# Optimization experiments

Hardware: AMD Instinct MI355X
Metric: run time of the kernel (lower is better)

## Reference

```python
import jax, jax.numpy as jnp
import numpy as np

B, S, D, H, DH = 4, 2048, 1024, 16, 64
INIT_STD = 0.02
IGNORE = -100000.0


def setup_inputs() -> dict:
    key = jax.random.key(0)
    ks = jax.random.split(key, 5)
    x = jax.random.normal(ks[0], (B, S, D), dtype=jnp.float32)
    W_Q = INIT_STD * jax.random.normal(ks[1], (H, D, DH), dtype=jnp.float32)
    W_K = INIT_STD * jax.random.normal(ks[2], (H, D, DH), dtype=jnp.float32)
    W_V = INIT_STD * jax.random.normal(ks[3], (H, D, DH), dtype=jnp.float32)
    W_O = INIT_STD * jax.random.normal(ks[4], (H, DH, D), dtype=jnp.float32)
    b_Q = jnp.zeros((H, DH), dtype=jnp.float32)
    b_K = jnp.zeros((H, DH), dtype=jnp.float32)
    b_V = jnp.zeros((H, DH), dtype=jnp.float32)
    b_O = jnp.zeros((D,), dtype=jnp.float32)
    return {"x": x, "W_Q": W_Q, "b_Q": b_Q, "W_K": W_K, "b_K": b_K,
            "W_V": W_V, "b_V": b_V, "W_O": W_O, "b_O": b_O}


def reference(x, W_Q, b_Q, W_K, b_K, W_V, b_V, W_O, b_O):
    # x: (B, S, D); projections -> (B, S, H, DH)
    Q = jnp.einsum('bqd,hde->bqhe', x, W_Q) + b_Q
    K = jnp.einsum('bkd,hde->bkhe', x, W_K) + b_K
    V = jnp.einsum('bkd,hde->bkhe', x, W_V) + b_V
    d_head = Q.shape[-1]
    # scores: (B, H, Sq, Sk)
    scores = jnp.einsum('bqhe,bkhe->bhqk', Q, K) / np.sqrt(d_head).astype(np.float32)
    s = scores.shape[-1]
    causal = jnp.triu(jnp.ones((s, s), dtype=bool), k=1)
    scores = jnp.where(causal, jnp.float32(IGNORE), scores)
    A = jax.nn.softmax(scores, axis=-1)
    z = jnp.einsum('bhqk,bkhe->bqhe', A, V)
    # output projection: sum over heads + bias
    attn_out = jnp.einsum('bqhe,hed->bqd', z, W_O) + b_O
    return attn_out
```

## Files before the change

kernel.cpp:

```cpp
#include <hip/hip_runtime.h>


#define B_ 4
#define S_ 2048
#define D_ 1024
#define H_ 16
#define DH_ 64

typedef unsigned short ushort_t;
typedef __attribute__((ext_vector_type(4))) short short4v;
typedef __attribute__((ext_vector_type(8))) short short8v;
typedef __attribute__((ext_vector_type(4))) float floatx4;
typedef __attribute__((ext_vector_type(4))) unsigned short ushort4v;

static __device__ __forceinline__ ushort_t f2bf(float f) {
    union { float f; unsigned u; } v; v.f = f;
    unsigned r = v.u + 0x7fffu + ((v.u >> 16) & 1u);
    return (ushort_t)(r >> 16);
}

static __device__ __forceinline__ float fast_exp2(float x) {
#if __has_builtin(__builtin_amdgcn_exp2f)
    return __builtin_amdgcn_exp2f(x);
#else
    return exp2f(x);
#endif
}

static __device__ __forceinline__ unsigned pack_bf16_tr(float lo, float hi) {
    union { float f; unsigned u; } a, b;
    a.f = lo; b.f = hi;
    return __builtin_amdgcn_perm(b.u, a.u, 0x07060302u);
}

static __device__ __forceinline__ void g2lds16(const void* g, void* l) {
    __builtin_amdgcn_global_load_lds(
        (__attribute__((address_space(1))) void*)(unsigned long long)(size_t)g,
        (__attribute__((address_space(3))) void*)(unsigned int)(size_t)l,
        16, 0, 0);
}

__global__ void prep_kernel(const float* __restrict__ x,
                            const float* __restrict__ wq, const float* __restrict__ wk,
                            const float* __restrict__ wv, const float* __restrict__ wo,
                            ushort_t* __restrict__ xb, ushort_t* __restrict__ wt,
                            ushort_t* __restrict__ wot) {
    __shared__ float tile[32][33];
    int bid = blockIdx.x;
    int tid = threadIdx.x;
    if (bid < 8192) {
        int i = (bid * 256 + tid) * 4;
        float4 v = *(const float4*)&x[i];
        ushort4v o;
        o[0] = f2bf(v.x); o[1] = f2bf(v.y); o[2] = f2bf(v.z); o[3] = f2bf(v.w);
        *(ushort4v*)&xb[i] = o;
        return;
    }
    const float* src;
    ushort_t* d;
    int C, r0, c0;
    if (bid < 11264) {
        int t = bid - 8192;
        int z = t / 64, r = t % 64;
        src = (z < 16 ? wq : (z < 32 ? wk : wv)) + (size_t)(z & 15) * 65536;
        d = wt + (size_t)z * 65536;
        C = 64; r0 = (r >> 1) * 32; c0 = (r & 1) * 32;
    } else {
        int t = bid - 11264;
        int z = t / 64, r = t % 64;
        src = wo + (size_t)z * 65536;
        d = wot + (size_t)z * 64;
        C = 1024; r0 = (r & 1) * 32; c0 = (r >> 1) * 32;
    }
    int tx = tid & 31, ty = tid >> 5;
#pragma unroll
    for (int i = 0; i < 4; ++i)
        tile[ty + i * 8][tx] = src[(size_t)(r0 + ty + i * 8) * C + c0 + tx];
    __syncthreads();
#pragma unroll
    for (int i = 0; i < 4; ++i)
        d[(size_t)(c0 + ty + i * 8) * 1024 + r0 + tx] = f2bf(tile[tx][ty + i * 8]);
}


#define GQ_BAR() __builtin_amdgcn_s_barrier()
#define GQ_VM4 do { asm volatile("s_waitcnt vmcnt(4)"); __builtin_amdgcn_sched_barrier(0); } while (0)
#define GQ_VM1 do { asm volatile("s_waitcnt vmcnt(1)"); __builtin_amdgcn_sched_barrier(0); } while (0)
#define GQ_VM0 do { asm volatile("s_waitcnt vmcnt(0)"); __builtin_amdgcn_sched_barrier(0); } while (0)
#define GQ_WAITLG do { asm volatile("s_waitcnt lgkmcnt(0)"); __builtin_amdgcn_sched_barrier(0); } while (0)

#define GQ_READS_B(KB)                                                          \
    _Pragma("unroll") for (int nt = 0; nt < 4; ++nt)                            \
        bfr[KB][nt] = *(const short8v*)&cB[(wn * 64 + nt * 16) * 64 + ((KB) ? kb1 : kb0)];

#define GQ_READS_A(MH, KB)                                                      \
    _Pragma("unroll") for (int i = 0; i < 2; ++i)                               \
        af[i] = *(const short8v*)&cA[(wm * 64 + ((MH) * 2 + i) * 16) * 64 + ((KB) ? kb1 : kb0)];

#define GQ_MFMA(MH, KB)                                                         \
    GQ_WAITLG;                                                                  \
    __builtin_amdgcn_s_setprio(1);                                              \
    _Pragma("unroll") for (int i = 0; i < 2; ++i)                               \
        _Pragma("unroll") for (int nt = 0; nt < 4; ++nt)                        \
            acc[(MH) * 2 + i][nt] = __builtin_amdgcn_mfma_f32_16x16x32_bf16(    \
                af[i], bfr[KB][nt], acc[(MH) * 2 + i][nt], 0, 0, 0);            \
    __builtin_amdgcn_s_setprio(0);                                              \
    __builtin_amdgcn_sched_barrier(0);

#define GQ_KSTEP(CA, CB, S1, S2, S3, S4, WMID, WEND) do {                       \
    const ushort_t* cA = (CA); const ushort_t* cB = (CB);                       \
    short8v af[2]; short8v bfr[2][4];                                           \
    GQ_READS_B(0) GQ_READS_A(0, 0) S1; GQ_BAR();                                \
    GQ_MFMA(0, 0) GQ_BAR();                                                     \
    GQ_READS_B(1) GQ_READS_A(0, 1) S2; GQ_BAR();                                \
    GQ_MFMA(0, 1) WMID; GQ_BAR();                                               \
    GQ_READS_A(1, 0) S3; GQ_BAR();                                              \
    GQ_MFMA(1, 0) GQ_BAR();                                                     \
    GQ_READS_A(1, 1) S4; GQ_BAR();                                              \
    GQ_MFMA(1, 1) WEND; GQ_BAR();                                               \
} while (0)

#define GQ_BODY(APTR, BPTR)                                                     \
    stageA1(sA[0], 0, uRA);                                                     \
    stageB1(sB[0], 0, w * 32);                                                  \
    stageB1(sB[0], 0, w * 32 + 8);                                              \
    stageB1(sB[0], 0, w * 32 + 16);                                             \
    stageB1(sB[0], 0, w * 32 + 24);                                             \
    stageA1(sA[0], 0, uRA + 32);                                                \
    GQ_VM1;                                                                     \
    GQ_BAR();                                                                   \
    int p = 0;                                                                  \
    for (int t = 0; t < 15; ++t) {                                              \
        const int kk = (t + 1) * 64;                                            \
        ushort_t* nA = sA[p ^ 1];                                               \
        ushort_t* nB = sB[p ^ 1];                                               \
        GQ_KSTEP(sA[p], sB[p],                                                  \
                 { stageA1(nA, kk, uRA); stageB1(nB, kk, w * 32); },            \
                 { stageB1(nB, kk, w * 32 + 8); stageB1(nB, kk, w * 32 + 16); },\
                 { stageB1(nB, kk, w * 32 + 24); },                             \
                 { stageA1(nA, kk, uRA + 32); },                                \
                 GQ_VM4, GQ_VM1);                                               \
        p ^= 1;                                                                 \
    }                                                                           \
    GQ_KSTEP(sA[1], sB[1], (void)0, (void)0, (void)0, (void)0, GQ_VM0, (void)0);

__global__ __launch_bounds__(512, 2) void gemm_qkv(const ushort_t* __restrict__ A,
                                                   const ushort_t* __restrict__ Wt,
                                                   const float* __restrict__ bq,
                                                   const float* __restrict__ bk,
                                                   const float* __restrict__ bv,
                                                   ushort_t* __restrict__ Qw,
                                                   ushort_t* __restrict__ Kw,
                                                   ushort_t* __restrict__ Vw) {
    __shared__ ushort_t sA[2][128 * 64];
    __shared__ ushort_t sB[2][256 * 64];
    const int tid = threadIdx.x;
    const int lane = tid & 63, w = tid >> 6;
    const int lq = lane & 15, quad = lane >> 4;
    const int wm = w >> 2, wn = w & 3;
    const int m0 = blockIdx.x * 128, n0 = blockIdx.y * 256;

    const int kb0 = lq * 64 + ((quad ^ (lq & 7)) << 3);
    const int kb1 = lq * 64 + (((4 | quad) ^ (lq & 7)) << 3);

    const int uRA = ((w >> 2) << 6) + (w & 3) * 8;

    auto stageA1 = [&](ushort_t* dst, int kk, int R0) __attribute__((always_inline)) {
        int rr = R0 + (lane >> 3);
        int cc = (lane & 7) ^ (rr & 7);
        g2lds16(&A[(size_t)(m0 + rr) * 1024 + kk + cc * 8], &dst[R0 * 64]);
    };
    auto stageB1 = [&](ushort_t* dst, int kk, int R0) __attribute__((always_inline)) {
        int rr = R0 + (lane >> 3);
        int cc = (lane & 7) ^ (rr & 7);
        g2lds16(&Wt[(size_t)(n0 + rr) * 1024 + kk + cc * 8], &dst[R0 * 64]);
    };

    floatx4 acc[4][4] = {};

    GQ_BODY(A, Wt)

    const int mat = blockIdx.y >> 2;
    const float* bias = mat == 0 ? bq : (mat == 1 ? bk : bv);
    const int colbase = (blockIdx.y & 3) * 256 + wn * 64;
    float bias_v[4];
#pragma unroll
    for (int nt = 0; nt < 4; ++nt) bias_v[nt] = bias[colbase + nt * 16 + lq];

#pragma unroll
    for (int mt = 0; mt < 4; ++mt) {
#pragma unroll
        for (int nt = 0; nt < 4; ++nt) {
            int row0 = m0 + wm * 64 + mt * 16 + quad * 4;
            int col = colbase + nt * 16 + lq;
            int h = col >> 6, e = col & 63;
            if (mat == 2) {
                int b = row0 >> 11, s = row0 & 2047;
                ushort4v pk;
#pragma unroll
                for (int rg = 0; rg < 4; ++rg) pk[rg] = f2bf(acc[mt][nt][rg] + bias_v[nt]);
                *(ushort4v*)&Vw[((size_t)((b << 4) | h) * 64 + e) * 2048 + s] = pk;
            } else {
                ushort_t* Du = mat == 0 ? Qw : Kw;
#pragma unroll
                for (int rg = 0; rg < 4; ++rg) {
                    int row = row0 + rg;
                    int b = row >> 11, s = row & 2047;
                    float v = acc[mt][nt][rg] + bias_v[nt];
                    if (mat == 0) v *= 0.18033688011112042f;
                    Du[((size_t)((b << 4) | h) * 2048 + s) * 64 + e] = f2bf(v);
                }
            }
        }
    }
}

#define VROW 140
__global__ __launch_bounds__(256, 3) void attn_kernel(const ushort_t* __restrict__ Q,
                                                      const ushort_t* __restrict__ Kg,
                                                      const ushort_t* __restrict__ Vt,
                                                      ushort_t* __restrict__ Z) {
    __shared__ ushort_t sK[2][128 * 64];
    __shared__ ushort_t sV[64 * VROW];
    const int tid = threadIdx.x;
    const int lane = tid & 63, w = tid >> 6;
    const int lq = lane & 15, quad = lane >> 4;
    const int bh = blockIdx.x;
    const int b = bh >> 4, h = bh & 15;
    const ushort_t* Qp = Q + (size_t)bh * S_ * DH_;
    const ushort_t* Kp = Kg + (size_t)bh * S_ * DH_;
    const ushort_t* Vp = Vt + (size_t)bh * DH_ * S_;

    const int kbase0 = lq * 64 + ((quad ^ (lq & 7)) << 3);
    const int kbase1 = lq * 64 + (((4 | quad) ^ (lq & 7)) << 3);
    const int vbase = lq * VROW + quad * 4;
    const int vr = w * 16 + (lane >> 2);
    const int vc = (lane & 3) * 32;

    const floatx4 fzero = {0.f, 0.f, 0.f, 0.f};

    auto stageK = [&](int kt, int bs) __attribute__((always_inline)) {
        ushort_t* dK = sK[bs];
#pragma unroll
        for (int p = 0; p < 4; ++p) {
            int rrk = w * 32 + p * 8 + (lane >> 3);
            int ck = (lane & 7) ^ (rrk & 7);
            g2lds16(&Kp[(size_t)(kt * 128 + rrk) * 64 + ck * 8], &dK[(w * 32 + p * 8) * 64]);
        }
    };
    auto loadV = [&](int kt, short8v* vr4) __attribute__((always_inline)) {
        const ushort_t* src = &Vp[(size_t)vr * 2048 + kt * 128 + vc];
#pragma unroll
        for (int j = 0; j < 4; ++j) vr4[j] = *(const short8v*)&src[j * 8];
    };
    auto writeV = [&](const short8v* vr4) __attribute__((always_inline)) {
        ushort_t* dst = &sV[vr * VROW + vc];
#pragma unroll
        for (int j = 0; j < 4; ++j) *(short8v*)&dst[j * 8] = vr4[j];
    };

    const int qt = 15 - (int)blockIdx.y;
    const int q0 = qt * 128;

    short8v qf[2][2];
#pragma unroll
    for (int qi = 0; qi < 2; ++qi)
#pragma unroll
        for (int ks = 0; ks < 2; ++ks)
            qf[qi][ks] = *(const short8v*)&Qp[(size_t)(q0 + w * 32 + qi * 16 + lq) * DH_ + ks * 32 + quad * 8];

    float l_i[2] = {0.f, 0.f};
    floatx4 o[2][4] = {};
    short8v vreg[4];

    stageK(0, 0);
    loadV(0, vreg);

    for (int kt = 0; kt <= qt; ++kt) {
        const bool diag = (kt == qt);
        const ushort_t* cK = sK[kt & 1];

        __syncthreads();
        writeV(vreg);
        if (kt < qt) {
            stageK(kt + 1, (kt + 1) & 1);
            loadV(kt + 1, vreg);
        }

        floatx4 st[8][2];
#pragma unroll
        for (int si = 0; si < 8; ++si) {
            short8v a0 = *(const short8v*)&cK[kbase0 + si * 1024];
            short8v a1 = *(const short8v*)&cK[kbase1 + si * 1024];
#pragma unroll
            for (int qi = 0; qi < 2; ++qi) {
                st[si][qi] = __builtin_amdgcn_mfma_f32_16x16x32_bf16(a0, qf[qi][0], fzero, 0, 0, 0);
                st[si][qi] = __builtin_amdgcn_mfma_f32_16x16x32_bf16(a1, qf[qi][1], st[si][qi], 0, 0, 0);
            }
        }

        short4v pf[8][2];
#pragma unroll
        for (int qi = 0; qi < 2; ++qi) {
            const int qg = q0 + w * 32 + qi * 16 + lq;
            float lsum = 0.f;
#pragma unroll
            for (int si = 0; si < 8; ++si) {
                float p[4];
#pragma unroll
                for (int rg = 0; rg < 4; ++rg) {
                    float v = st[si][qi][rg];
                    if (diag) {
                        int sg = kt * 128 + si * 16 + quad * 4 + rg;
                        if (sg > qg) v = -1e30f;
                    }
                    p[rg] = fast_exp2(v);
                    lsum += p[rg];
                }
                union { unsigned u[2]; short4v v4; } pk;
                pk.u[0] = pack_bf16_tr(p[0], p[1]);
                pk.u[1] = pack_bf16_tr(p[2], p[3]);
                pf[si][qi] = pk.v4;
            }
            l_i[qi] += lsum;
        }

        __syncthreads();

#pragma unroll
        for (int ksp = 0; ksp < 8; ++ksp) {
#pragma unroll
            for (int et = 0; et < 4; ++et) {
                short4v vf = *(const short4v*)&sV[vbase + et * (16 * VROW) + ksp * 16];
#pragma unroll
                for (int qi = 0; qi < 2; ++qi)
                    o[qi][et] = __builtin_amdgcn_mfma_f32_16x16x16bf16_1k(pf[ksp][qi], vf, o[qi][et], 0, 0, 0);
            }
        }
    }

#pragma unroll
    for (int qi = 0; qi < 2; ++qi) {
        float lf = l_i[qi];
        lf += __shfl_xor(lf, 16);
        lf += __shfl_xor(lf, 32);
        float linv[4];
#pragma unroll
        for (int rg = 0; rg < 4; ++rg) linv[rg] = 1.0f / __shfl(lf, quad * 4 + rg);
#pragma unroll
        for (int et = 0; et < 4; ++et) {
#pragma unroll
            for (int rg = 0; rg < 4; ++rg) {
                int qg = q0 + w * 32 + qi * 16 + quad * 4 + rg;
                int e = et * 16 + lq;
                Z[((size_t)(b * S_ + qg) * H_ + h) * DH_ + e] = f2bf(o[qi][et][rg] * linv[rg]);
            }
        }
    }
}

__global__ __launch_bounds__(512, 2) void gemm_o(const ushort_t* __restrict__ A,
                                                 const ushort_t* __restrict__ Bt,
                                                 const float* __restrict__ bias,
                                                 float* __restrict__ Dst) {
    __shared__ ushort_t sA[2][128 * 64];
    __shared__ ushort_t sB[2][256 * 64];
    const int tid = threadIdx.x;
    const int lane = tid & 63, w = tid >> 6;
    const int lq = lane & 15, quad = lane >> 4;
    const int wm = w >> 2, wn = w & 3;
    const int m0 = blockIdx.x * 128, n0 = blockIdx.y * 256;

    const int kb0 = lq * 64 + ((quad ^ (lq & 7)) << 3);
    const int kb1 = lq * 64 + (((4 | quad) ^ (lq & 7)) << 3);
    const int uRA = ((w >> 2) << 6) + (w & 3) * 8;

    auto stageA1 = [&](ushort_t* dst, int kk, int R0) __attribute__((always_inline)) {
        int rr = R0 + (lane >> 3);
        int cc = (lane & 7) ^ (rr & 7);
        g2lds16(&A[(size_t)(m0 + rr) * 1024 + kk + cc * 8], &dst[R0 * 64]);
    };
    auto stageB1 = [&](ushort_t* dst, int kk, int R0) __attribute__((always_inline)) {
        int rr = R0 + (lane >> 3);
        int cc = (lane & 7) ^ (rr & 7);
        g2lds16(&Bt[(size_t)(n0 + rr) * 1024 + kk + cc * 8], &dst[R0 * 64]);
    };

    floatx4 acc[4][4] = {};

    GQ_BODY(A, Bt)

    const int colbase = n0 + wn * 64;
    float bias_v[4];
#pragma unroll
    for (int nt = 0; nt < 4; ++nt) bias_v[nt] = bias[colbase + nt * 16 + lq];

#pragma unroll
    for (int mt = 0; mt < 4; ++mt) {
#pragma unroll
        for (int nt = 0; nt < 4; ++nt) {
            int row0 = m0 + wm * 64 + mt * 16 + quad * 4;
            int col = colbase + nt * 16 + lq;
#pragma unroll
            for (int rg = 0; rg < 4; ++rg)
                Dst[(size_t)(row0 + rg) * 1024 + col] = acc[mt][nt][rg] + bias_v[nt];
        }
    }
}

extern "C" void kernel_launch(void* const* d_in, const int* in_sizes, int n_in,
                              void* d_out, int out_size, void* d_ws, size_t ws_size,
                              hipStream_t stream) {
    const float* x  = (const float*)d_in[0];
    const float* wq = (const float*)d_in[1];
    const float* bq = (const float*)d_in[2];
    const float* wk = (const float*)d_in[3];
    const float* bk = (const float*)d_in[4];
    const float* wv = (const float*)d_in[5];
    const float* bv = (const float*)d_in[6];
    const float* wo = (const float*)d_in[7];
    const float* bo = (const float*)d_in[8];

    char* ws = (char*)d_ws;
    size_t off = 0;
    ushort_t* xb  = (ushort_t*)(ws + off); off += (size_t)8192 * 1024 * 2;
    ushort_t* wt  = (ushort_t*)(ws + off); off += (size_t)3 * 1024 * 1024 * 2;
    ushort_t* wot = (ushort_t*)(ws + off); off += (size_t)1024 * 1024 * 2;
    ushort_t* Qw  = (ushort_t*)(ws + off); off += (size_t)8192 * 1024 * 2;
    ushort_t* Kw  = (ushort_t*)(ws + off); off += (size_t)8192 * 1024 * 2;
    ushort_t* Vw  = (ushort_t*)(ws + off); off += (size_t)8192 * 1024 * 2;
    ushort_t* Zw  = (ushort_t*)(ws + off); off += (size_t)8192 * 1024 * 2;

    prep_kernel<<<12288, 256, 0, stream>>>(x, wq, wk, wv, wo, xb, wt, wot);
    gemm_qkv<<<dim3(64, 12), 512, 0, stream>>>(xb, wt, bq, bk, bv, Qw, Kw, Vw);
    attn_kernel<<<dim3(64, 16), 256, 0, stream>>>(Qw, Kw, Vw, Zw);
    gemm_o<<<dim3(64, 4), 512, 0, stream>>>(Zw, wot, bo, (float*)d_out);
}
```

Measured before the change: 295.8 us.

## Shrink GEMM tiles to 128x128 and pair causal query tiles in attention

Both projection GEMMs move from 512-thread 128x256 tiles to 256-thread 128x128 tiles, doubling the grid and adjusting the staging and waitcnt bookkeeping. The attention kernel now processes two complementary query tiles per block (qt and 15-qt) to balance causal work, halving the grid. V is staged through async global-to-LDS copies into a double-buffered, XOR-swizzled layout instead of a register round trip into a padded array, which removes one barrier per iteration. The changes trade per-block work size and occupancy against load balance and more tile-level reuse of global loads.

```diff
diff --git a/kernel.cpp b/kernel.cpp
--- a/kernel.cpp
+++ b/kernel.cpp
@@ -85,7 +85,7 @@
 
 #define GQ_BAR() __builtin_amdgcn_s_barrier()
 #define GQ_VM4 do { asm volatile("s_waitcnt vmcnt(4)"); __builtin_amdgcn_sched_barrier(0); } while (0)
-#define GQ_VM1 do { asm volatile("s_waitcnt vmcnt(1)"); __builtin_amdgcn_sched_barrier(0); } while (0)
+#define GQ_VM2 do { asm volatile("s_waitcnt vmcnt(2)"); __builtin_amdgcn_sched_barrier(0); } while (0)
 #define GQ_VM0 do { asm volatile("s_waitcnt vmcnt(0)"); __builtin_amdgcn_sched_barrier(0); } while (0)
 #define GQ_WAITLG do { asm volatile("s_waitcnt lgkmcnt(0)"); __builtin_amdgcn_sched_barrier(0); } while (0)
 
@@ -120,14 +120,12 @@
     GQ_MFMA(1, 1) WEND; GQ_BAR();                                               \
 } while (0)
 
-#define GQ_BODY(APTR, BPTR)                                                     \
-    stageA1(sA[0], 0, uRA);                                                     \
-    stageB1(sB[0], 0, w * 32);                                                  \
-    stageB1(sB[0], 0, w * 32 + 8);                                              \
-    stageB1(sB[0], 0, w * 32 + 16);                                             \
-    stageB1(sB[0], 0, w * 32 + 24);                                             \
-    stageA1(sA[0], 0, uRA + 32);                                                \
-    GQ_VM1;                                                                     \
+#define GQ_RUN()                                                                \
+    stA(sA[0], 0, uA); stA(sA[0], 0, uA + 8);                                   \
+    stB(sB[0], 0, bR); stB(sB[0], 0, bR + 8);                                   \
+    stB(sB[0], 0, bR + 16); stB(sB[0], 0, bR + 24);                             \
+    stA(sA[0], 0, uA + 32); stA(sA[0], 0, uA + 40);                             \
+    GQ_VM2;                                                                     \
     GQ_BAR();                                                                   \
     int p = 0;                                                                  \
     for (int t = 0; t < 15; ++t) {                                              \
@@ -135,16 +133,16 @@
         ushort_t* nA = sA[p ^ 1];                                               \
         ushort_t* nB = sB[p ^ 1];                                               \
         GQ_KSTEP(sA[p], sB[p],                                                  \
-                 { stageA1(nA, kk, uRA); stageB1(nB, kk, w * 32); },            \
-                 { stageB1(nB, kk, w * 32 + 8); stageB1(nB, kk, w * 32 + 16); },\
-                 { stageB1(nB, kk, w * 32 + 24); },                             \
-                 { stageA1(nA, kk, uRA + 32); },                                \
-                 GQ_VM4, GQ_VM1);                                               \
+                 { stA(nA, kk, uA); stA(nA, kk, uA + 8); },                     \
+                 { stB(nB, kk, bR); stB(nB, kk, bR + 8); },                     \
+                 { stB(nB, kk, bR + 16); stB(nB, kk, bR + 24); },               \
+                 { stA(nA, kk, uA + 32); stA(nA, kk, uA + 40); },               \
+                 GQ_VM4, GQ_VM2);                                               \
         p ^= 1;                                                                 \
     }                                                                           \
     GQ_KSTEP(sA[1], sB[1], (void)0, (void)0, (void)0, (void)0, GQ_VM0, (void)0);
 
-__global__ __launch_bounds__(512, 2) void gemm_qkv(const ushort_t* __restrict__ A,
+__global__ __launch_bounds__(256, 2) void gemm_qkv(const ushort_t* __restrict__ A,
                                                    const ushort_t* __restrict__ Wt,
                                                    const float* __restrict__ bq,
                                                    const float* __restrict__ bk,
@@ -153,24 +151,25 @@
                                                    ushort_t* __restrict__ Kw,
                                                    ushort_t* __restrict__ Vw) {
     __shared__ ushort_t sA[2][128 * 64];
-    __shared__ ushort_t sB[2][256 * 64];
+    __shared__ ushort_t sB[2][128 * 64];
     const int tid = threadIdx.x;
     const int lane = tid & 63, w = tid >> 6;
     const int lq = lane & 15, quad = lane >> 4;
-    const int wm = w >> 2, wn = w & 3;
-    const int m0 = blockIdx.x * 128, n0 = blockIdx.y * 256;
+    const int wm = w >> 1, wn = w & 1;
+    const int m0 = blockIdx.x * 128, n0 = blockIdx.y * 128;
 
     const int kb0 = lq * 64 + ((quad ^ (lq & 7)) << 3);
     const int kb1 = lq * 64 + (((4 | quad) ^ (lq & 7)) << 3);
 
-    const int uRA = ((w >> 2) << 6) + (w & 3) * 8;
-
-    auto stageA1 = [&](ushort_t* dst, int kk, int R0) __attribute__((always_inline)) {
+    const int uA = ((w >> 1) << 6) + ((w & 1) << 4);
+    const int bR = w * 32;
+
+    auto stA = [&](ushort_t* dst, int kk, int R0) __attribute__((always_inline)) {
         int rr = R0 + (lane >> 3);
         int cc = (lane & 7) ^ (rr & 7);
         g2lds16(&A[(size_t)(m0 + rr) * 1024 + kk + cc * 8], &dst[R0 * 64]);
     };
-    auto stageB1 = [&](ushort_t* dst, int kk, int R0) __attribute__((always_inline)) {
+    auto stB = [&](ushort_t* dst, int kk, int R0) __attribute__((always_inline)) {
         int rr = R0 + (lane >> 3);
         int cc = (lane & 7) ^ (rr & 7);
         g2lds16(&Wt[(size_t)(n0 + rr) * 1024 + kk + cc * 8], &dst[R0 * 64]);
@@ -178,11 +177,11 @@
 
     floatx4 acc[4][4] = {};
 
-    GQ_BODY(A, Wt)
-
-    const int mat = blockIdx.y >> 2;
+    GQ_RUN()
+
+    const int mat = blockIdx.y >> 3;
     const float* bias = mat == 0 ? bq : (mat == 1 ? bk : bv);
-    const int colbase = (blockIdx.y & 3) * 256 + wn * 64;
+    const int colbase = (blockIdx.y & 7) * 128 + wn * 64;
     float bias_v[4];
 #pragma unroll
     for (int nt = 0; nt < 4; ++nt) bias_v[nt] = bias[colbase + nt * 16 + lq];
@@ -215,13 +214,12 @@
     }
 }
 
-#define VROW 140
-__global__ __launch_bounds__(256, 3) void attn_kernel(const ushort_t* __restrict__ Q,
-                                                      const ushort_t* __restrict__ Kg,
-                                                      const ushort_t* __restrict__ Vt,
-                                                      ushort_t* __restrict__ Z) {
+__global__ __launch_bounds__(256) void attn_kernel(const ushort_t* __restrict__ Q,
+                                                   const ushort_t* __restrict__ Kg,
+                                                   const ushort_t* __restrict__ Vt,
+                                                   ushort_t* __restrict__ Z) {
     __shared__ ushort_t sK[2][128 * 64];
-    __shared__ ushort_t sV[64 * VROW];
+    __shared__ ushort_t sV[2][64 * 128];
     const int tid = threadIdx.x;
     const int lane = tid & 63, w = tid >> 6;
     const int lq = lane & 15, quad = lane >> 4;
@@ -233,9 +231,8 @@
 
     const int kbase0 = lq * 64 + ((quad ^ (lq & 7)) << 3);
     const int kbase1 = lq * 64 + (((4 | quad) ^ (lq & 7)) << 3);
-    const int vbase = lq * VROW + quad * 4;
-    const int vr = w * 16 + (lane >> 2);
-    const int vc = (lane & 3) * 32;
+    const int vbase2 = lq * 128 + quad * 4;
+    const int vko = (lq & 7) << 4;
 
     const floatx4 fzero = {0.f, 0.f, 0.f, 0.f};
 
@@ -248,139 +245,142 @@
             g2lds16(&Kp[(size_t)(kt * 128 + rrk) * 64 + ck * 8], &dK[(w * 32 + p * 8) * 64]);
         }
     };
-    auto loadV = [&](int kt, short8v* vr4) __attribute__((always_inline)) {
-        const ushort_t* src = &Vp[(size_t)vr * 2048 + kt * 128 + vc];
-#pragma unroll
-        for (int j = 0; j < 4; ++j) vr4[j] = *(const short8v*)&src[j * 8];
-    };
-    auto writeV = [&](const short8v* vr4) __attribute__((always_inline)) {
-        ushort_t* dst = &sV[vr * VROW + vc];
-#pragma unroll
-        for (int j = 0; j < 4; ++j) *(short8v*)&dst[j * 8] = vr4[j];
-    };
-
-    const int qt = 15 - (int)blockIdx.y;
-    const int q0 = qt * 128;
-
-    short8v qf[2][2];
-#pragma unroll
-    for (int qi = 0; qi < 2; ++qi)
-#pragma unroll
-        for (int ks = 0; ks < 2; ++ks)
-            qf[qi][ks] = *(const short8v*)&Qp[(size_t)(q0 + w * 32 + qi * 16 + lq) * DH_ + ks * 32 + quad * 8];
-
-    float l_i[2] = {0.f, 0.f};
-    floatx4 o[2][4] = {};
-    short8v vreg[4];
-
-    stageK(0, 0);
-    loadV(0, vreg);
-
-    for (int kt = 0; kt <= qt; ++kt) {
-        const bool diag = (kt == qt);
-        const ushort_t* cK = sK[kt & 1];
+    auto stageV = [&](int kt, int bs) __attribute__((always_inline)) {
+        ushort_t* dV = sV[bs];
+#pragma unroll
+        for (int p = 0; p < 4; ++p) {
+            int R0 = w * 16 + p * 4;
+            int e = R0 + (lane >> 4);
+            int u = lane & 15;
+            int usw = ((((u >> 1) ^ (e & 7)) << 1) | (u & 1));
+            g2lds16(&Vp[(size_t)e * 2048 + kt * 128 + usw * 8], &dV[R0 * 128]);
+        }
+    };
+
+    for (int pass = 0; pass < 2; ++pass) {
+        const int qt = pass == 0 ? (int)blockIdx.y : 15 - (int)blockIdx.y;
+        const int q0 = qt * 128;
+
+        short8v qf[2][2];
+#pragma unroll
+        for (int qi = 0; qi < 2; ++qi)
+#pragma unroll
+            for (int ks = 0; ks < 2; ++ks)
+                qf[qi][ks] = *(const short8v*)&Qp[(size_t)(q0 + w * 32 + qi * 16 + lq) * DH_ + ks * 32 + quad * 8];
+
+        float l_i[2] = {0.f, 0.f};
+        floatx4 o[2][4] = {};
 
         __syncthreads();
-        writeV(vreg);
-        if (kt < qt) {
-            stageK(kt + 1, (kt + 1) & 1);
-            loadV(kt + 1, vreg);
-        }
-
-        floatx4 st[8][2];
-#pragma unroll
-        for (int si = 0; si < 8; ++si) {
-            short8v a0 = *(const short8v*)&cK[kbase0 + si * 1024];
-            short8v a1 = *(const short8v*)&cK[kbase1 + si * 1024];
+        stageK(0, 0);
+        stageV(0, 0);
+
+        for (int kt = 0; kt <= qt; ++kt) {
+            const bool diag = (kt == qt);
+            const ushort_t* cK = sK[kt & 1];
+            const ushort_t* cV = sV[kt & 1];
+
+            __syncthreads();
+            if (kt < qt) {
+                stageK(kt + 1, (kt + 1) & 1);
+                stageV(kt + 1, (kt + 1) & 1);
+            }
+
+            floatx4 st[8][2];
+#pragma unroll
+            for (int si = 0; si < 8; ++si) {
+                short8v a0 = *(const short8v*)&cK[kbase0 + si * 1024];
+                short8v a1 = *(const short8v*)&cK[kbase1 + si * 1024];
+#pragma unroll
+                for (int qi = 0; qi < 2; ++qi) {
+                    st[si][qi] = __builtin_amdgcn_mfma_f32_16x16x32_bf16(a0, qf[qi][0], fzero, 0, 0, 0);
+                    st[si][qi] = __builtin_amdgcn_mfma_f32_16x16x32_bf16(a1, qf[qi][1], st[si][qi], 0, 0, 0);
+                }
+            }
+
+            short4v pf[8][2];
 #pragma unroll
             for (int qi = 0; qi < 2; ++qi) {
-                st[si][qi] = __builtin_amdgcn_mfma_f32_16x16x32_bf16(a0, qf[qi][0], fzero, 0, 0, 0);
-                st[si][qi] = __builtin_amdgcn_mfma_f32_16x16x32_bf16(a1, qf[qi][1], st[si][qi], 0, 0, 0);
-            }
-        }
-
-        short4v pf[8][2];
+                const int qg = q0 + w * 32 + qi * 16 + lq;
+                float lsum = 0.f;
+#pragma unroll
+                for (int si = 0; si < 8; ++si) {
+                    float p[4];
+#pragma unroll
+                    for (int rg = 0; rg < 4; ++rg) {
+                        float v = st[si][qi][rg];
+                        if (diag) {
+                            int sg = kt * 128 + si * 16 + quad * 4 + rg;
+                            if (sg > qg) v = -1e30f;
+                        }
+                        p[rg] = fast_exp2(v);
+                        lsum += p[rg];
+                    }
+                    union { unsigned u[2]; short4v v4; } pk;
+                    pk.u[0] = pack_bf16_tr(p[0], p[1]);
+                    pk.u[1] = pack_bf16_tr(p[2], p[3]);
+                    pf[si][qi] = pk.v4;
+                }
+                l_i[qi] += lsum;
+            }
+
+#pragma unroll
+            for (int ksp = 0; ksp < 8; ++ksp) {
+                const ushort_t* pV = &cV[vbase2 + ((ksp << 4) ^ vko)];
+#pragma unroll
+                for (int et = 0; et < 4; ++et) {
+                    short4v vf = *(const short4v*)&pV[et * 2048];
+#pragma unroll
+                    for (int qi = 0; qi < 2; ++qi)
+                        o[qi][et] = __builtin_amdgcn_mfma_f32_16x16x16bf16_1k(pf[ksp][qi], vf, o[qi][et], 0, 0, 0);
+                }
+            }
+        }
+
 #pragma unroll
         for (int qi = 0; qi < 2; ++qi) {
-            const int qg = q0 + w * 32 + qi * 16 + lq;
-            float lsum = 0.f;
-#pragma unroll
-            for (int si = 0; si < 8; ++si) {
-                float p[4];
+            float lf = l_i[qi];
+            lf += __shfl_xor(lf, 16);
+            lf += __shfl_xor(lf, 32);
+            float linv[4];
+#pragma unroll
+            for (int rg = 0; rg < 4; ++rg) linv[rg] = 1.0f / __shfl(lf, quad * 4 + rg);
+#pragma unroll
+            for (int et = 0; et < 4; ++et) {
 #pragma unroll
                 for (int rg = 0; rg < 4; ++rg) {
-                    float v = st[si][qi][rg];
-                    if (diag) {
-                        int sg = kt * 128 + si * 16 + quad * 4 + rg;
-                        if (sg > qg) v = -1e30f;
-                    }
-                    p[rg] = fast_exp2(v);
-                    lsum += p[rg];
+                    int qg = q0 + w * 32 + qi * 16 + quad * 4 + rg;
+                    int e = et * 16 + lq;
+                    Z[((size_t)(b * S_ + qg) * H_ + h) * DH_ + e] = f2bf(o[qi][et][rg] * linv[rg]);
                 }
-                union { unsigned u[2]; short4v v4; } pk;
-                pk.u[0] = pack_bf16_tr(p[0], p[1]);
-                pk.u[1] = pack_bf16_tr(p[2], p[3]);
-                pf[si][qi] = pk.v4;
-            }
-            l_i[qi] += lsum;
-        }
-
-        __syncthreads();
-
-#pragma unroll
-        for (int ksp = 0; ksp < 8; ++ksp) {
-#pragma unroll
-            for (int et = 0; et < 4; ++et) {
-                short4v vf = *(const short4v*)&sV[vbase + et * (16 * VROW) + ksp * 16];
-#pragma unroll
-                for (int qi = 0; qi < 2; ++qi)
-                    o[qi][et] = __builtin_amdgcn_mfma_f32_16x16x16bf16_1k(pf[ksp][qi], vf, o[qi][et], 0, 0, 0);
             }
         }
     }
-
-#pragma unroll
-    for (int qi = 0; qi < 2; ++qi) {
-        float lf = l_i[qi];
-        lf += __shfl_xor(lf, 16);
-        lf += __shfl_xor(lf, 32);
-        float linv[4];
-#pragma unroll
-        for (int rg = 0; rg < 4; ++rg) linv[rg] = 1.0f / __shfl(lf, quad * 4 + rg);
-#pragma unroll
-        for (int et = 0; et < 4; ++et) {
-#pragma unroll
-            for (int rg = 0; rg < 4; ++rg) {
-                int qg = q0 + w * 32 + qi * 16 + quad * 4 + rg;
-                int e = et * 16 + lq;
-                Z[((size_t)(b * S_ + qg) * H_ + h) * DH_ + e] = f2bf(o[qi][et][rg] * linv[rg]);
-            }
-        }
-    }
-}
-
-__global__ __launch_bounds__(512, 2) void gemm_o(const ushort_t* __restrict__ A,
+}
+
+__global__ __launch_bounds__(256, 2) void gemm_o(const ushort_t* __restrict__ A,
                                                  const ushort_t* __restrict__ Bt,
                                                  const float* __restrict__ bias,
                                                  float* __restrict__ Dst) {
     __shared__ ushort_t sA[2][128 * 64];
-    __shared__ ushort_t sB[2][256 * 64];
+    __shared__ ushort_t sB[2][128 * 64];
     const int tid = threadIdx.x;
     const int lane = tid & 63, w = tid >> 6;
     const int lq = lane & 15, quad = lane >> 4;
-    const int wm = w >> 2, wn = w & 3;
-    const int m0 = blockIdx.x * 128, n0 = blockIdx.y * 256;
+    const int wm = w >> 1, wn = w & 1;
+    const int m0 = blockIdx.x * 128, n0 = blockIdx.y * 128;
 
     const int kb0 = lq * 64 + ((quad ^ (lq & 7)) << 3);
     const int kb1 = lq * 64 + (((4 | quad) ^ (lq & 7)) << 3);
-    const int uRA = ((w >> 2) << 6) + (w & 3) * 8;
-
-    auto stageA1 = [&](ushort_t* dst, int kk, int R0) __attribute__((always_inline)) {
+    const int uA = ((w >> 1) << 6) + ((w & 1) << 4);
+    const int bR = w * 32;
+
+    auto stA = [&](ushort_t* dst, int kk, int R0) __attribute__((always_inline)) {
         int rr = R0 + (lane >> 3);
         int cc = (lane & 7) ^ (rr & 7);
         g2lds16(&A[(size_t)(m0 + rr) * 1024 + kk + cc * 8], &dst[R0 * 64]);
     };
-    auto stageB1 = [&](ushort_t* dst, int kk, int R0) __attribute__((always_inline)) {
+    auto stB = [&](ushort_t* dst, int kk, int R0) __attribute__((always_inline)) {
         int rr = R0 + (lane >> 3);
         int cc = (lane & 7) ^ (rr & 7);
         g2lds16(&Bt[(size_t)(n0 + rr) * 1024 + kk + cc * 8], &dst[R0 * 64]);
@@ -388,7 +388,7 @@
 
     floatx4 acc[4][4] = {};
 
-    GQ_BODY(A, Bt)
+    GQ_RUN()
 
     const int colbase = n0 + wn * 64;
     float bias_v[4];
@@ -432,7 +432,7 @@
     ushort_t* Zw  = (ushort_t*)(ws + off); off += (size_t)8192 * 1024 * 2;
 
     prep_kernel<<<12288, 256, 0, stream>>>(x, wq, wk, wv, wo, xb, wt, wot);
-    gemm_qkv<<<dim3(64, 12), 512, 0, stream>>>(xb, wt, bq, bk, bv, Qw, Kw, Vw);
-    attn_kernel<<<dim3(64, 16), 256, 0, stream>>>(Qw, Kw, Vw, Zw);
-    gemm_o<<<dim3(64, 4), 512, 0, stream>>>(Zw, wot, bo, (float*)d_out);
-}
+    gemm_qkv<<<dim3(64, 24), 256, 0, stream>>>(xb, wt, bq, bk, bv, Qw, Kw, Vw);
+    attn_kernel<<<dim3(64, 8), 256, 0, stream>>>(Qw, Kw, Vw, Zw);
+    gemm_o<<<dim3(64, 8), 256, 0, stream>>>(Zw, wot, bo, (float*)d_out);
+}
```

New measurement: 246.7 us (median of 3 runs). 16.6% less time.
